# Kernel optimization log

Hardware: AMD Instinct MI355X
Metric: run time of the kernel (lower is better)

Reference implementation:

```python
import jax, jax.numpy as jnp
import numpy as np

N = 100000          # num nodes
NUM_GRAPHS = 64
NEG_SLOPE = 0.2     # PyG GATv2Conv default


def gatv2_layer(x, src, dst, Wl, bl, Wr, br, att, bias, heads, out_ch, concat):
    # x: [N, F_in]; src/dst: [E] (self-loops already included)
    xl = (x @ Wl + bl).reshape(-1, heads, out_ch)   # source transform
    xr = (x @ Wr + br).reshape(-1, heads, out_ch)   # target transform
    m = jax.nn.leaky_relu(xl[src] + xr[dst], NEG_SLOPE)      # [E, H, C]
    alpha = jnp.einsum('ehc,hc->eh', m, att)                 # [E, H]
    # segment softmax over destination nodes
    amax = jax.ops.segment_max(alpha, dst, num_segments=N)
    alpha = jnp.exp(alpha - amax[dst])
    denom = jax.ops.segment_sum(alpha, dst, num_segments=N)
    alpha = alpha / (denom[dst] + 1e-16)
    out = jax.ops.segment_sum(xl[src] * alpha[..., None], dst, num_segments=N)
    out = out.reshape(N, heads * out_ch) if concat else out.mean(axis=1)
    return out + bias


def setup_inputs() -> dict:
    key = jax.random.key(0)
    ks = jax.random.split(key, 16)
    E = 3200000
    x = jax.random.normal(ks[0], (N, 256), dtype=jnp.float32)
    edge_index = jax.random.randint(ks[1], (2, E), 0, N, dtype=jnp.int64)
    batch = jnp.sort(jax.random.randint(ks[2], (N,), 0, NUM_GRAPHS, dtype=jnp.int64))
    H1, C1 = 8, 4
    s1 = 1.0 / np.sqrt(256)
    s2 = 1.0 / np.sqrt(H1 * C1)
    return {
        'x': x, 'edge_index': edge_index, 'batch': batch,
        'W1l': jax.random.normal(ks[3], (256, H1 * C1), jnp.float32) * s1,
        'b1l': jnp.zeros((H1 * C1,), jnp.float32),
        'W1r': jax.random.normal(ks[4], (256, H1 * C1), jnp.float32) * s1,
        'b1r': jnp.zeros((H1 * C1,), jnp.float32),
        'att1': jax.random.normal(ks[5], (H1, C1), jnp.float32),
        'bias1': jnp.zeros((H1 * C1,), jnp.float32),
        'W2l': jax.random.normal(ks[6], (H1 * C1, 64), jnp.float32) * s2,
        'b2l': jnp.zeros((64,), jnp.float32),
        'W2r': jax.random.normal(ks[7], (H1 * C1, 64), jnp.float32) * s2,
        'b2r': jnp.zeros((64,), jnp.float32),
        'att2': jax.random.normal(ks[8], (1, 64), jnp.float32),
        'bias2': jnp.zeros((64,), jnp.float32),
    }


def reference(x, edge_index, batch, W1l, b1l, W1r, b1r, att1, bias1,
              W2l, b2l, W2r, b2r, att2, bias2):
    # add self-loops (PyG GATv2Conv default add_self_loops=True)
    loop = jnp.arange(N, dtype=edge_index.dtype)
    src = jnp.concatenate([edge_index[0], loop])
    dst = jnp.concatenate([edge_index[1], loop])
    h = gatv2_layer(x, src, dst, W1l, b1l, W1r, b1r, att1, bias1, 8, 4, True)
    h = jax.nn.elu(h)
    h = gatv2_layer(h, src, dst, W2l, b2l, W2r, b2r, att2, bias2, 1, 64, False)
    # global mean pool over graphs
    sums = jax.ops.segment_sum(h, batch, num_segments=NUM_GRAPHS)
    counts = jax.ops.segment_sum(jnp.ones((N, 1), h.dtype), batch, num_segments=NUM_GRAPHS)
    return sums / jnp.maximum(counts, 1.0)
```

## Files before the change

kernel.cpp:

```cpp
#include <hip/hip_runtime.h>
#include <math.h>

#define NN 100000
#define EE 3200000
#define ET (EE + NN)
#define NG 64

#define NB 196
#define BWID 512
#define PCHUNK 8192
#define PBLOCKS ((ET + PCHUNK - 1) / PCHUNK)

#define OFF_XL1B  0u
#define OFF_XR1   1600000u
#define OFF_H     4800000u
#define OFF_HL2B  8000000u
#define OFF_HR2   11200000u
#define OFF_BEDGE 8000000u
#define OFF_RP    17600000u
#define OFF_ESRC  17700096u
#define OFF_POOL  21000096u
#define OFF_CNTG  21004192u
#define OFF_BCNT  21004256u
#define OFF_BOFF  21004512u
#define OFF_GCUR  21004768u
#define WS_UNITS  21005024u

__device__ __forceinline__ float lrelu(float v) { return v > 0.0f ? v : 0.2f * v; }

__device__ __forceinline__ unsigned pack_bf2(float a, float b) {
  unsigned ua = __float_as_uint(a), ub = __float_as_uint(b);
  ua = (ua + 0x7FFFu + ((ua >> 16) & 1u)) >> 16;
  ub = (ub + 0x7FFFu + ((ub >> 16) & 1u)) & 0xFFFF0000u;
  return ua | ub;
}
__device__ __forceinline__ float bf_lo(unsigned u) { return __uint_as_float(u << 16); }
__device__ __forceinline__ float bf_hi(unsigned u) { return __uint_as_float(u & 0xFFFF0000u); }

__global__ __launch_bounds__(256) void k_bcount(const int* __restrict__ ei,
                                                int* __restrict__ bcnt) {
  __shared__ int h[NB];
  for (int i = threadIdx.x; i < NB; i += 256) h[i] = 0;
  __syncthreads();
  for (long e = (long)blockIdx.x * 256 + threadIdx.x; e < ET; e += (long)gridDim.x * 256) {
    int d = (e < EE) ? ei[EE + e] : (int)(e - EE);
    atomicAdd(&h[d >> 9], 1);
  }
  __syncthreads();
  for (int i = threadIdx.x; i < NB; i += 256) if (h[i]) atomicAdd(&bcnt[i], h[i]);
}

__global__ __launch_bounds__(256) void k_bscan(const int* __restrict__ bcnt,
                                               int* __restrict__ boff, int* __restrict__ gcur) {
  __shared__ int sd[256];
  int t = threadIdx.x;
  int v = (t < NB) ? bcnt[t] : 0;
  sd[t] = v;
  __syncthreads();
  for (int o = 1; o < 256; o <<= 1) {
    int u = (t >= o) ? sd[t - o] : 0;
    __syncthreads();
    sd[t] += u;
    __syncthreads();
  }
  if (t < NB) { boff[t] = sd[t] - v; gcur[t] = sd[t] - v; }
  if (t == 0) boff[NB] = ET;
}

__global__ __launch_bounds__(512) void k_part(const int* __restrict__ ei,
                                              int* __restrict__ gcur,
                                              int* __restrict__ bedge) {
  __shared__ int  cnt[NB];
  __shared__ int  lbase[NB];
  __shared__ int  gbase[NB];
  __shared__ int  sc[256];
  __shared__ int  buf[PCHUNK];
  __shared__ unsigned char bkt[PCHUNK];
  int tid = threadIdx.x;
  long e0 = (long)blockIdx.x * PCHUNK;
  int nedge = (e0 + PCHUNK <= ET) ? PCHUNK : (int)(ET - e0);

  for (int i = tid; i < NB; i += 512) cnt[i] = 0;
  __syncthreads();
  for (int i = tid; i < nedge; i += 512) {
    long e = e0 + i;
    int d = (e < EE) ? ei[EE + e] : (int)(e - EE);
    atomicAdd(&cnt[d >> 9], 1);
  }
  __syncthreads();
  if (tid < 256) sc[tid] = (tid < NB) ? cnt[tid] : 0;
  __syncthreads();
  for (int o = 1; o < 256; o <<= 1) {
    int u = (tid < 256 && tid >= o) ? sc[tid - o] : 0;
    __syncthreads();
    if (tid < 256) sc[tid] += u;
    __syncthreads();
  }
  if (tid < NB) lbase[tid] = sc[tid] - cnt[tid];
  __syncthreads();
  if (tid < NB) {
    int c = cnt[tid];
    gbase[tid] = c ? atomicAdd(&gcur[tid], c) : 0;
    cnt[tid] = 0;
  }
  __syncthreads();
  for (int i = tid; i < nedge; i += 512) {
    long e = e0 + i;
    int s, d;
    if (e < EE) { s = ei[e]; d = ei[EE + e]; }
    else { s = (int)(e - EE); d = s; }
    int b = d >> 9;
    int r = atomicAdd(&cnt[b], 1);
    int idx = lbase[b] + r;
    buf[idx] = s | ((d & 511) << 17);
    bkt[idx] = (unsigned char)b;
  }
  __syncthreads();
  for (int i = tid; i < nedge; i += 512) {
    int p = buf[i];
    int b = bkt[i];
    bedge[gbase[b] + (i - lbase[b])] = p;
  }
}

__global__ __launch_bounds__(512) void k_csr(const int* __restrict__ boff,
                                             const int* __restrict__ bedge,
                                             int* __restrict__ rp, int* __restrict__ esrc) {
  __shared__ int sdeg[BWID];
  __shared__ int sscan[BWID];
  int b = blockIdx.x, t = threadIdx.x;
  int n0 = b * BWID;
  int lo = boff[b], hi = boff[b + 1];
  sdeg[t] = 0;
  __syncthreads();
  for (int i = lo + t; i < hi; i += 512) {
    int p = bedge[i];
    atomicAdd(&sdeg[p >> 17], 1);
  }
  __syncthreads();
  int v = sdeg[t];
  sscan[t] = v;
  __syncthreads();
  for (int o = 1; o < 512; o <<= 1) {
    int u = (t >= o) ? sscan[t - o] : 0;
    __syncthreads();
    sscan[t] += u;
    __syncthreads();
  }
  int excl = sscan[t] - v;
  int n = n0 + t;
  if (n < NN) rp[n] = lo + excl;
  if (b == NB - 1 && t == 0) rp[NN] = ET;
  __syncthreads();
  sdeg[t] = lo + excl;
  __syncthreads();
  for (int i = lo + t; i < hi; i += 512) {
    int p = bedge[i];
    int pos = atomicAdd(&sdeg[p >> 17], 1);
    esrc[pos] = p & 0x1FFFF;
  }
}

#define FMA4A(a, xv) \
  a.x += xv.x*w0.x + xv.y*w1.x + xv.z*w2.x + xv.w*w3.x; \
  a.y += xv.x*w0.y + xv.y*w1.y + xv.z*w2.y + xv.w*w3.y; \
  a.z += xv.x*w0.z + xv.y*w1.z + xv.z*w2.z + xv.w*w3.z; \
  a.w += xv.x*w0.w + xv.y*w1.w + xv.z*w2.w + xv.w*w3.w;

__global__ __launch_bounds__(256, 4) void k_xform1(
    const float* __restrict__ x,
    const float* __restrict__ Wl, const float* __restrict__ bl,
    const float* __restrict__ Wr, const float* __restrict__ br,
    unsigned short* __restrict__ xl1b, float* __restrict__ xr1) {
  __shared__ float Wlds[64 * 64];
  int tid = threadIdx.x;
  int ci = tid & 15, ni = tid >> 4;
  int cbase = ci * 4;
  int n0 = blockIdx.x * 64 + ni * 4;
  int r0 = n0 + 0 < NN ? n0 + 0 : NN - 1;
  int r1 = n0 + 1 < NN ? n0 + 1 : NN - 1;
  int r2 = n0 + 2 < NN ? n0 + 2 : NN - 1;
  int r3 = n0 + 3 < NN ? n0 + 3 : NN - 1;
  const float* xb0 = x + (size_t)r0 * 256;
  const float* xb1 = x + (size_t)r1 * 256;
  const float* xb2 = x + (size_t)r2 * 256;
  const float* xb3 = x + (size_t)r3 * 256;
  float4 acc0 = {0,0,0,0}, acc1 = {0,0,0,0}, acc2 = {0,0,0,0}, acc3 = {0,0,0,0};

  for (int q = 0; q < 4; ++q) {
    int k0 = q * 64;
    __syncthreads();
    for (int i = tid; i < 64 * 64; i += 256) {
      int k = (i >> 6) + k0, c = i & 63;
      Wlds[i] = (c < 32) ? Wl[k * 32 + c] : Wr[k * 32 + (c - 32)];
    }
    __syncthreads();
#pragma unroll 2
    for (int kk = 0; kk < 64; kk += 4) {
      int k = k0 + kk;
      float4 xv0 = *(const float4*)(xb0 + k);
      float4 xv1 = *(const float4*)(xb1 + k);
      float4 xv2 = *(const float4*)(xb2 + k);
      float4 xv3 = *(const float4*)(xb3 + k);
      const float* wr = &Wlds[kk * 64 + cbase];
      float4 w0 = *(const float4*)(wr);
      float4 w1 = *(const float4*)(wr + 64);
      float4 w2 = *(const float4*)(wr + 128);
      float4 w3 = *(const float4*)(wr + 192);
      FMA4A(acc0, xv0)
      FMA4A(acc1, xv1)
      FMA4A(acc2, xv2)
      FMA4A(acc3, xv3)
    }
  }
  float4 acc[4] = {acc0, acc1, acc2, acc3};
  if (cbase < 32) {
    float4 bv = { bl[cbase], bl[cbase+1], bl[cbase+2], bl[cbase+3] };
#pragma unroll
    for (int j = 0; j < 4; ++j) {
      int n = n0 + j;
      if (n < NN) {
        uint2 o = { pack_bf2(acc[j].x + bv.x, acc[j].y + bv.y),
                    pack_bf2(acc[j].z + bv.z, acc[j].w + bv.w) };
        *(uint2*)(xl1b + (size_t)n * 32 + cbase) = o;
      }
    }
  } else {
    int c2 = cbase - 32;
    float4 bv = { br[c2], br[c2+1], br[c2+2], br[c2+3] };
#pragma unroll
    for (int j = 0; j < 4; ++j) {
      int n = n0 + j;
      if (n < NN) {
        float4 o = { acc[j].x + bv.x, acc[j].y + bv.y, acc[j].z + bv.z, acc[j].w + bv.w };
        *(float4*)(xr1 + (size_t)n * 32 + c2) = o;
      }
    }
  }
}

__global__ __launch_bounds__(256) void k_gather1(
    const int* __restrict__ rp, const int* __restrict__ esrc,
    const unsigned short* __restrict__ xl1b, const float* __restrict__ xr1,
    const float* __restrict__ att1, const float* __restrict__ bias1,
    float* __restrict__ h) {
  int n = blockIdx.x * 8 + (threadIdx.x >> 5);
  if (n >= NN) return;
  int l = threadIdx.x & 31;
  float av = att1[l];
  float xr = xr1[(size_t)n * 32 + l];
  int rpn = rp[n], dg = rp[n + 1] - rpn;
  float acc = 0.0f, den = 0.0f;
  int j = 0;
  for (; j + 4 <= dg; j += 4) {
    int s0 = esrc[rpn + j + 0];
    int s1 = esrc[rpn + j + 1];
    int s2 = esrc[rpn + j + 2];
    int s3 = esrc[rpn + j + 3];
    float x0 = bf_lo(xl1b[(size_t)s0 * 32 + l]);
    float x1 = bf_lo(xl1b[(size_t)s1 * 32 + l]);
    float x2 = bf_lo(xl1b[(size_t)s2 * 32 + l]);
    float x3 = bf_lo(xl1b[(size_t)s3 * 32 + l]);
    float p0 = lrelu(x0 + xr) * av;
    float p1 = lrelu(x1 + xr) * av;
    float p2 = lrelu(x2 + xr) * av;
    float p3 = lrelu(x3 + xr) * av;
    p0 += __shfl_xor(p0, 1); p1 += __shfl_xor(p1, 1);
    p2 += __shfl_xor(p2, 1); p3 += __shfl_xor(p3, 1);
    p0 += __shfl_xor(p0, 2); p1 += __shfl_xor(p1, 2);
    p2 += __shfl_xor(p2, 2); p3 += __shfl_xor(p3, 2);
    float w0 = __expf(p0), w1 = __expf(p1), w2 = __expf(p2), w3 = __expf(p3);
    den += w0 + w1 + w2 + w3;
    acc += w0 * x0 + w1 * x1 + w2 * x2 + w3 * x3;
  }
  for (; j < dg; ++j) {
    int s = esrc[rpn + j];
    float xl = bf_lo(xl1b[(size_t)s * 32 + l]);
    float p = lrelu(xl + xr) * av;
    p += __shfl_xor(p, 1);
    p += __shfl_xor(p, 2);
    float w = __expf(p);
    den += w;
    acc += w * xl;
  }
  float v = acc / (den + 1e-16f) + bias1[l];
  h[(size_t)n * 32 + l] = v > 0.0f ? v : expm1f(v);
}

__global__ __launch_bounds__(256) void k_xform2(
    const float* __restrict__ h,
    const float* __restrict__ Wl, const float* __restrict__ bl,
    const float* __restrict__ Wr, const float* __restrict__ br,
    unsigned short* __restrict__ hl2b, float* __restrict__ hr2) {
  __shared__ float Wlds[32 * 128];
  int tid = threadIdx.x;
  for (int i = tid; i < 32 * 128; i += 256) {
    int k = i >> 7, c = i & 127;
    Wlds[i] = (c < 64) ? Wl[k * 64 + c] : Wr[k * 64 + (c - 64)];
  }
  __syncthreads();
  int ci = tid & 31, ni = tid >> 5;
  int cbase = ci * 4;
  int n0 = blockIdx.x * 32 + ni * 4;
  const float* hb0 = h + (size_t)(n0 + 0) * 32;
  const float* hb1 = h + (size_t)(n0 + 1) * 32;
  const float* hb2 = h + (size_t)(n0 + 2) * 32;
  const float* hb3 = h + (size_t)(n0 + 3) * 32;
  float4 acc0 = {0,0,0,0}, acc1 = {0,0,0,0}, acc2 = {0,0,0,0}, acc3 = {0,0,0,0};
#pragma unroll
  for (int k = 0; k < 32; k += 4) {
    float4 xv0 = *(const float4*)(hb0 + k);
    float4 xv1 = *(const float4*)(hb1 + k);
    float4 xv2 = *(const float4*)(hb2 + k);
    float4 xv3 = *(const float4*)(hb3 + k);
    const float* wr = &Wlds[k * 128 + cbase];
    float4 w0 = *(const float4*)(wr);
    float4 w1 = *(const float4*)(wr + 128);
    float4 w2 = *(const float4*)(wr + 256);
    float4 w3 = *(const float4*)(wr + 384);
    FMA4A(acc0, xv0)
    FMA4A(acc1, xv1)
    FMA4A(acc2, xv2)
    FMA4A(acc3, xv3)
  }
  float4 acc[4] = {acc0, acc1, acc2, acc3};
  if (cbase < 64) {
    float4 bv = { bl[cbase], bl[cbase+1], bl[cbase+2], bl[cbase+3] };
#pragma unroll
    for (int j = 0; j < 4; ++j) {
      uint2 o = { pack_bf2(acc[j].x + bv.x, acc[j].y + bv.y),
                  pack_bf2(acc[j].z + bv.z, acc[j].w + bv.w) };
      *(uint2*)(hl2b + (size_t)(n0 + j) * 64 + cbase) = o;
    }
  } else {
    int c2 = cbase - 64;
    float4 bv = { br[c2], br[c2+1], br[c2+2], br[c2+3] };
#pragma unroll
    for (int j = 0; j < 4; ++j) {
      float4 o = { acc[j].x + bv.x, acc[j].y + bv.y, acc[j].z + bv.z, acc[j].w + bv.w };
      *(float4*)(hr2 + (size_t)(n0 + j) * 64 + c2) = o;
    }
  }
}

__global__ __launch_bounds__(256) void k_gather2(
    const int* __restrict__ rp, const int* __restrict__ esrc,
    const unsigned short* __restrict__ hl2b, const float* __restrict__ hr2,
    const float* __restrict__ att2, const float* __restrict__ bias2,
    const int* __restrict__ batch,
    float* __restrict__ pool, float* __restrict__ cntg) {
  __shared__ float ssum[4][64];
  __shared__ float scnt[4];
  int tid = threadIdx.x;
  int n = (blockIdx.x * 256 + tid) >> 3;
  int l8 = tid & 7;
  int nblk0 = blockIdx.x * 32;
  int gmin = batch[nblk0];
  int gspan = batch[nblk0 + 31] - gmin + 1;
  ssum[tid >> 6][tid & 63] = 0.0f;
  if (tid < 4) scnt[tid] = 0.0f;
  __syncthreads();

  float4 ac0 = *(const float4*)(att2 + l8 * 8);
  float4 ac1 = *(const float4*)(att2 + l8 * 8 + 4);
  float4 bs0 = *(const float4*)(bias2 + l8 * 8);
  float4 bs1 = *(const float4*)(bias2 + l8 * 8 + 4);
  const float4* hrp = (const float4*)(hr2 + (size_t)n * 64 + l8 * 8);
  float4 hr0 = hrp[0], hr1 = hrp[1];
  int rpn = rp[n], dg = rp[n + 1] - rpn;
  float4 a0 = {0,0,0,0}, a1 = {0,0,0,0};
  float den = 0.0f;
  int j = 0;
  for (; j + 2 <= dg; j += 2) {
    int s0 = esrc[rpn + j];
    int s1 = esrc[rpn + j + 1];
    uint4 q0 = *(const uint4*)(hl2b + (size_t)s0 * 64 + l8 * 8);
    uint4 q1 = *(const uint4*)(hl2b + (size_t)s1 * 64 + l8 * 8);
    float4 u0 = { bf_lo(q0.x), bf_hi(q0.x), bf_lo(q0.y), bf_hi(q0.y) };
    float4 u1 = { bf_lo(q0.z), bf_hi(q0.z), bf_lo(q0.w), bf_hi(q0.w) };
    float4 v0 = { bf_lo(q1.x), bf_hi(q1.x), bf_lo(q1.y), bf_hi(q1.y) };
    float4 v1 = { bf_lo(q1.z), bf_hi(q1.z), bf_lo(q1.w), bf_hi(q1.w) };
    float p0 = lrelu(u0.x + hr0.x) * ac0.x + lrelu(u0.y + hr0.y) * ac0.y
             + lrelu(u0.z + hr0.z) * ac0.z + lrelu(u0.w + hr0.w) * ac0.w
             + lrelu(u1.x + hr1.x) * ac1.x + lrelu(u1.y + hr1.y) * ac1.y
             + lrelu(u1.z + hr1.z) * ac1.z + lrelu(u1.w + hr1.w) * ac1.w;
    float p1 = lrelu(v0.x + hr0.x) * ac0.x + lrelu(v0.y + hr0.y) * ac0.y
             + lrelu(v0.z + hr0.z) * ac0.z + lrelu(v0.w + hr0.w) * ac0.w
             + lrelu(v1.x + hr1.x) * ac1.x + lrelu(v1.y + hr1.y) * ac1.y
             + lrelu(v1.z + hr1.z) * ac1.z + lrelu(v1.w + hr1.w) * ac1.w;
    p0 += __shfl_xor(p0, 1); p1 += __shfl_xor(p1, 1);
    p0 += __shfl_xor(p0, 2); p1 += __shfl_xor(p1, 2);
    p0 += __shfl_xor(p0, 4); p1 += __shfl_xor(p1, 4);
    float w0 = __expf(p0), w1 = __expf(p1);
    den += w0 + w1;
    a0.x += w0 * u0.x + w1 * v0.x; a0.y += w0 * u0.y + w1 * v0.y;
    a0.z += w0 * u0.z + w1 * v0.z; a0.w += w0 * u0.w + w1 * v0.w;
    a1.x += w0 * u1.x + w1 * v1.x; a1.y += w0 * u1.y + w1 * v1.y;
    a1.z += w0 * u1.z + w1 * v1.z; a1.w += w0 * u1.w + w1 * v1.w;
  }
  for (; j < dg; ++j) {
    int s = esrc[rpn + j];
    uint4 q0 = *(const uint4*)(hl2b + (size_t)s * 64 + l8 * 8);
    float4 u0 = { bf_lo(q0.x), bf_hi(q0.x), bf_lo(q0.y), bf_hi(q0.y) };
    float4 u1 = { bf_lo(q0.z), bf_hi(q0.z), bf_lo(q0.w), bf_hi(q0.w) };
    float p = lrelu(u0.x + hr0.x) * ac0.x + lrelu(u0.y + hr0.y) * ac0.y
            + lrelu(u0.z + hr0.z) * ac0.z + lrelu(u0.w + hr0.w) * ac0.w
            + lrelu(u1.x + hr1.x) * ac1.x + lrelu(u1.y + hr1.y) * ac1.y
            + lrelu(u1.z + hr1.z) * ac1.z + lrelu(u1.w + hr1.w) * ac1.w;
    p += __shfl_xor(p, 1);
    p += __shfl_xor(p, 2);
    p += __shfl_xor(p, 4);
    float w = __expf(p);
    den += w;
    a0.x += w * u0.x; a0.y += w * u0.y; a0.z += w * u0.z; a0.w += w * u0.w;
    a1.x += w * u1.x; a1.y += w * u1.y; a1.z += w * u1.z; a1.w += w * u1.w;
  }
  float inv = 1.0f / (den + 1e-16f);
  int gi = batch[n] - gmin;
  float* sp = &ssum[gi][l8 * 8];
  atomicAdd(sp + 0, a0.x * inv + bs0.x);
  atomicAdd(sp + 1, a0.y * inv + bs0.y);
  atomicAdd(sp + 2, a0.z * inv + bs0.z);
  atomicAdd(sp + 3, a0.w * inv + bs0.w);
  atomicAdd(sp + 4, a1.x * inv + bs1.x);
  atomicAdd(sp + 5, a1.y * inv + bs1.y);
  atomicAdd(sp + 6, a1.z * inv + bs1.z);
  atomicAdd(sp + 7, a1.w * inv + bs1.w);
  if (l8 == 0) atomicAdd(&scnt[gi], 1.0f);
  __syncthreads();
  for (int i = tid; i < gspan * 64; i += 256)
    atomicAdd(pool + (size_t)(gmin + (i >> 6)) * 64 + (i & 63), ssum[i >> 6][i & 63]);
  if (tid < gspan) atomicAdd(cntg + gmin + tid, scnt[tid]);
}

__global__ __launch_bounds__(256) void k_final(
    const float* __restrict__ pool, const float* __restrict__ cntg,
    float* __restrict__ out) {
  int i = blockIdx.x * 256 + threadIdx.x;
  if (i < NG * 64) out[i] = pool[i] / fmaxf(cntg[i >> 6], 1.0f);
}

extern "C" void kernel_launch(void* const* d_in, const int* in_sizes, int n_in,
                              void* d_out, int out_size, void* d_ws, size_t ws_size,
                              hipStream_t stream) {
  const float* x     = (const float*)d_in[0];
  const int*   ei    = (const int*)d_in[1];
  const int*   batch = (const int*)d_in[2];
  const float* W1l   = (const float*)d_in[3];
  const float* b1l   = (const float*)d_in[4];
  const float* W1r   = (const float*)d_in[5];
  const float* b1r   = (const float*)d_in[6];
  const float* att1  = (const float*)d_in[7];
  const float* bias1 = (const float*)d_in[8];
  const float* W2l   = (const float*)d_in[9];
  const float* b2l   = (const float*)d_in[10];
  const float* W2r   = (const float*)d_in[11];
  const float* b2r   = (const float*)d_in[12];
  const float* att2  = (const float*)d_in[13];
  const float* bias2 = (const float*)d_in[14];
  float* ws = (float*)d_ws;
  int*   wi = (int*)d_ws;
  float* out = (float*)d_out;

  hipMemsetAsync(ws + OFF_POOL, 0, (size_t)(WS_UNITS - OFF_POOL) * 4, stream);

  k_bcount<<<512, 256, 0, stream>>>(ei, wi + OFF_BCNT);
  k_bscan<<<1, 256, 0, stream>>>(wi + OFF_BCNT, wi + OFF_BOFF, wi + OFF_GCUR);
  k_part<<<PBLOCKS, 512, 0, stream>>>(ei, wi + OFF_GCUR, wi + OFF_BEDGE);
  k_csr<<<NB, 512, 0, stream>>>(wi + OFF_BOFF, wi + OFF_BEDGE,
                                wi + OFF_RP, wi + OFF_ESRC);

  k_xform1<<<(NN + 63) / 64, 256, 0, stream>>>(x, W1l, b1l, W1r, b1r,
                                               (unsigned short*)(ws + OFF_XL1B), ws + OFF_XR1);
  k_gather1<<<NN / 8, 256, 0, stream>>>(wi + OFF_RP, wi + OFF_ESRC,
                                        (const unsigned short*)(ws + OFF_XL1B), ws + OFF_XR1,
                                        att1, bias1, ws + OFF_H);
  k_xform2<<<NN / 32, 256, 0, stream>>>(ws + OFF_H, W2l, b2l, W2r, b2r,
                                        (unsigned short*)(ws + OFF_HL2B), ws + OFF_HR2);
  k_gather2<<<(NN * 8 + 255) / 256, 256, 0, stream>>>(wi + OFF_RP, wi + OFF_ESRC,
                                                      (const unsigned short*)(ws + OFF_HL2B),
                                                      ws + OFF_HR2, att2, bias2, batch,
                                                      ws + OFF_POOL, ws + OFF_CNTG);
  k_final<<<16, 256, 0, stream>>>(ws + OFF_POOL, ws + OFF_CNTG, out);
}
```

Baseline: 383.9 us.

## Co-schedule layer-1 transform with CSR build kernels and unroll gather2 by four

Splits the first-layer node transform into two halves and runs them inside the edge-partition and CSR-build kernels as extra blocks, dispatched on block index with dynamic shared memory. The memory-bound dense transform then overlaps with the atomics-heavy graph construction instead of running as a separate launch afterwards. The transform now uses 512-thread blocks covering 128 nodes, and the shared-memory size is set by the larger partition role, which may reduce occupancy. Separately, the layer-2 gather loop is unrolled from two to four edges to expose more independent loads in flight.

Result: faster. 355.7 us (-7.3%).

```diff
diff --git a/kernel.cpp b/kernel.cpp
--- a/kernel.cpp
+++ b/kernel.cpp
@@ -10,6 +10,10 @@
 #define BWID 512
 #define PCHUNK 8192
 #define PBLOCKS ((ET + PCHUNK - 1) / PCHUNK)
+
+#define X1_SPLIT 50048
+#define X1BLK_A 391
+#define X1BLK_B 391
 
 #define OFF_XL1B  0u
 #define OFF_XR1   1600000u
@@ -67,17 +71,16 @@
   if (t == 0) boff[NB] = ET;
 }
 
-__global__ __launch_bounds__(512) void k_part(const int* __restrict__ ei,
-                                              int* __restrict__ gcur,
-                                              int* __restrict__ bedge) {
-  __shared__ int  cnt[NB];
-  __shared__ int  lbase[NB];
-  __shared__ int  gbase[NB];
-  __shared__ int  sc[256];
-  __shared__ int  buf[PCHUNK];
-  __shared__ unsigned char bkt[PCHUNK];
+__device__ void part_role(char* smem, const int* __restrict__ ei,
+                          int* __restrict__ gcur, int* __restrict__ bedge, int pblk) {
+  int* cnt   = (int*)smem;
+  int* lbase = cnt + NB;
+  int* gbase = lbase + NB;
+  int* sc    = gbase + NB;
+  int* buf   = sc + 256;
+  unsigned char* bkt = (unsigned char*)(buf + PCHUNK);
   int tid = threadIdx.x;
-  long e0 = (long)blockIdx.x * PCHUNK;
+  long e0 = (long)pblk * PCHUNK;
   int nedge = (e0 + PCHUNK <= ET) ? PCHUNK : (int)(ET - e0);
 
   for (int i = tid; i < NB; i += 512) cnt[i] = 0;
@@ -123,12 +126,12 @@
   }
 }
 
-__global__ __launch_bounds__(512) void k_csr(const int* __restrict__ boff,
-                                             const int* __restrict__ bedge,
-                                             int* __restrict__ rp, int* __restrict__ esrc) {
-  __shared__ int sdeg[BWID];
-  __shared__ int sscan[BWID];
-  int b = blockIdx.x, t = threadIdx.x;
+__device__ void csr_role(char* smem, const int* __restrict__ boff,
+                         const int* __restrict__ bedge,
+                         int* __restrict__ rp, int* __restrict__ esrc, int b) {
+  int* sdeg  = (int*)smem;
+  int* sscan = sdeg + BWID;
+  int t = threadIdx.x;
   int n0 = b * BWID;
   int lo = boff[b], hi = boff[b + 1];
   sdeg[t] = 0;
@@ -167,16 +170,16 @@
   a.z += xv.x*w0.z + xv.y*w1.z + xv.z*w2.z + xv.w*w3.z; \
   a.w += xv.x*w0.w + xv.y*w1.w + xv.z*w2.w + xv.w*w3.w;
 
-__global__ __launch_bounds__(256, 4) void k_xform1(
-    const float* __restrict__ x,
-    const float* __restrict__ Wl, const float* __restrict__ bl,
-    const float* __restrict__ Wr, const float* __restrict__ br,
-    unsigned short* __restrict__ xl1b, float* __restrict__ xr1) {
-  __shared__ float Wlds[64 * 64];
+__device__ void xform1_role(char* smem, const float* __restrict__ x,
+                            const float* __restrict__ Wl, const float* __restrict__ bl,
+                            const float* __restrict__ Wr, const float* __restrict__ br,
+                            unsigned short* __restrict__ xl1b, float* __restrict__ xr1,
+                            int n_base) {
+  float* Wlds = (float*)smem;
   int tid = threadIdx.x;
-  int ci = tid & 15, ni = tid >> 4;
+  int ci = tid & 15;
   int cbase = ci * 4;
-  int n0 = blockIdx.x * 64 + ni * 4;
+  int n0 = n_base + (tid >> 4) * 4;
   int r0 = n0 + 0 < NN ? n0 + 0 : NN - 1;
   int r1 = n0 + 1 < NN ? n0 + 1 : NN - 1;
   int r2 = n0 + 2 < NN ? n0 + 2 : NN - 1;
@@ -190,7 +193,7 @@
   for (int q = 0; q < 4; ++q) {
     int k0 = q * 64;
     __syncthreads();
-    for (int i = tid; i < 64 * 64; i += 256) {
+    for (int i = tid; i < 64 * 64; i += 512) {
       int k = (i >> 6) + k0, c = i & 63;
       Wlds[i] = (c < 32) ? Wl[k * 32 + c] : Wr[k * 32 + (c - 32)];
     }
@@ -237,6 +240,34 @@
       }
     }
   }
+}
+
+__global__ __launch_bounds__(512) void k_part_x1(
+    const int* __restrict__ ei, int* __restrict__ gcur, int* __restrict__ bedge,
+    const float* __restrict__ x,
+    const float* __restrict__ Wl, const float* __restrict__ bl,
+    const float* __restrict__ Wr, const float* __restrict__ br,
+    unsigned short* __restrict__ xl1b, float* __restrict__ xr1) {
+  extern __shared__ char smem[];
+  if (blockIdx.x < PBLOCKS)
+    part_role(smem, ei, gcur, bedge, blockIdx.x);
+  else
+    xform1_role(smem, x, Wl, bl, Wr, br, xl1b, xr1, (blockIdx.x - PBLOCKS) * 128);
+}
+
+__global__ __launch_bounds__(512) void k_csr_x1(
+    const int* __restrict__ boff, const int* __restrict__ bedge,
+    int* __restrict__ rp, int* __restrict__ esrc,
+    const float* __restrict__ x,
+    const float* __restrict__ Wl, const float* __restrict__ bl,
+    const float* __restrict__ Wr, const float* __restrict__ br,
+    unsigned short* __restrict__ xl1b, float* __restrict__ xr1) {
+  extern __shared__ char smem[];
+  if (blockIdx.x < NB)
+    csr_role(smem, boff, bedge, rp, esrc, blockIdx.x);
+  else
+    xform1_role(smem, x, Wl, bl, Wr, br, xl1b, xr1,
+                X1_SPLIT + (blockIdx.x - NB) * 128);
 }
 
 __global__ __launch_bounds__(256) void k_gather1(
@@ -343,6 +374,20 @@
   }
 }
 
+#define G2_P(qq, pp) { \
+  float4 U0 = { bf_lo(qq.x), bf_hi(qq.x), bf_lo(qq.y), bf_hi(qq.y) }; \
+  float4 U1 = { bf_lo(qq.z), bf_hi(qq.z), bf_lo(qq.w), bf_hi(qq.w) }; \
+  pp = lrelu(U0.x + hr0.x) * ac0.x + lrelu(U0.y + hr0.y) * ac0.y \
+     + lrelu(U0.z + hr0.z) * ac0.z + lrelu(U0.w + hr0.w) * ac0.w \
+     + lrelu(U1.x + hr1.x) * ac1.x + lrelu(U1.y + hr1.y) * ac1.y \
+     + lrelu(U1.z + hr1.z) * ac1.z + lrelu(U1.w + hr1.w) * ac1.w; }
+
+#define G2_ACC(qq, ww) { \
+  float4 U0 = { bf_lo(qq.x), bf_hi(qq.x), bf_lo(qq.y), bf_hi(qq.y) }; \
+  float4 U1 = { bf_lo(qq.z), bf_hi(qq.z), bf_lo(qq.w), bf_hi(qq.w) }; \
+  a0.x += ww * U0.x; a0.y += ww * U0.y; a0.z += ww * U0.z; a0.w += ww * U0.w; \
+  a1.x += ww * U1.x; a1.y += ww * U1.y; a1.z += ww * U1.z; a1.w += ww * U1.w; }
+
 __global__ __launch_bounds__(256) void k_gather2(
     const int* __restrict__ rp, const int* __restrict__ esrc,
     const unsigned short* __restrict__ hl2b, const float* __restrict__ hr2,
@@ -371,49 +416,38 @@
   float4 a0 = {0,0,0,0}, a1 = {0,0,0,0};
   float den = 0.0f;
   int j = 0;
-  for (; j + 2 <= dg; j += 2) {
-    int s0 = esrc[rpn + j];
+  for (; j + 4 <= dg; j += 4) {
+    int s0 = esrc[rpn + j + 0];
     int s1 = esrc[rpn + j + 1];
+    int s2 = esrc[rpn + j + 2];
+    int s3 = esrc[rpn + j + 3];
     uint4 q0 = *(const uint4*)(hl2b + (size_t)s0 * 64 + l8 * 8);
     uint4 q1 = *(const uint4*)(hl2b + (size_t)s1 * 64 + l8 * 8);
-    float4 u0 = { bf_lo(q0.x), bf_hi(q0.x), bf_lo(q0.y), bf_hi(q0.y) };
-    float4 u1 = { bf_lo(q0.z), bf_hi(q0.z), bf_lo(q0.w), bf_hi(q0.w) };
-    float4 v0 = { bf_lo(q1.x), bf_hi(q1.x), bf_lo(q1.y), bf_hi(q1.y) };
-    float4 v1 = { bf_lo(q1.z), bf_hi(q1.z), bf_lo(q1.w), bf_hi(q1.w) };
-    float p0 = lrelu(u0.x + hr0.x) * ac0.x + lrelu(u0.y + hr0.y) * ac0.y
-             + lrelu(u0.z + hr0.z) * ac0.z + lrelu(u0.w + hr0.w) * ac0.w
-             + lrelu(u1.x + hr1.x) * ac1.x + lrelu(u1.y + hr1.y) * ac1.y
-             + lrelu(u1.z + hr1.z) * ac1.z + lrelu(u1.w + hr1.w) * ac1.w;
-    float p1 = lrelu(v0.x + hr0.x) * ac0.x + lrelu(v0.y + hr0.y) * ac0.y
-             + lrelu(v0.z + hr0.z) * ac0.z + lrelu(v0.w + hr0.w) * ac0.w
-             + lrelu(v1.x + hr1.x) * ac1.x + lrelu(v1.y + hr1.y) * ac1.y
-             + lrelu(v1.z + hr1.z) * ac1.z + lrelu(v1.w + hr1.w) * ac1.w;
+    uint4 q2 = *(const uint4*)(hl2b + (size_t)s2 * 64 + l8 * 8);
+    uint4 q3 = *(const uint4*)(hl2b + (size_t)s3 * 64 + l8 * 8);
+    float p0, p1, p2, p3;
+    G2_P(q0, p0) G2_P(q1, p1) G2_P(q2, p2) G2_P(q3, p3)
     p0 += __shfl_xor(p0, 1); p1 += __shfl_xor(p1, 1);
+    p2 += __shfl_xor(p2, 1); p3 += __shfl_xor(p3, 1);
     p0 += __shfl_xor(p0, 2); p1 += __shfl_xor(p1, 2);
+    p2 += __shfl_xor(p2, 2); p3 += __shfl_xor(p3, 2);
     p0 += __shfl_xor(p0, 4); p1 += __shfl_xor(p1, 4);
-    float w0 = __expf(p0), w1 = __expf(p1);
-    den += w0 + w1;
-    a0.x += w0 * u0.x + w1 * v0.x; a0.y += w0 * u0.y + w1 * v0.y;
-    a0.z += w0 * u0.z + w1 * v0.z; a0.w += w0 * u0.w + w1 * v0.w;
-    a1.x += w0 * u1.x + w1 * v1.x; a1.y += w0 * u1.y + w1 * v1.y;
-    a1.z += w0 * u1.z + w1 * v1.z; a1.w += w0 * u1.w + w1 * v1.w;
+    p2 += __shfl_xor(p2, 4); p3 += __shfl_xor(p3, 4);
+    float w0 = __expf(p0), w1 = __expf(p1), w2 = __expf(p2), w3 = __expf(p3);
+    den += w0 + w1 + w2 + w3;
+    G2_ACC(q0, w0) G2_ACC(q1, w1) G2_ACC(q2, w2) G2_ACC(q3, w3)
   }
   for (; j < dg; ++j) {
     int s = esrc[rpn + j];
     uint4 q0 = *(const uint4*)(hl2b + (size_t)s * 64 + l8 * 8);
-    float4 u0 = { bf_lo(q0.x), bf_hi(q0.x), bf_lo(q0.y), bf_hi(q0.y) };
-    float4 u1 = { bf_lo(q0.z), bf_hi(q0.z), bf_lo(q0.w), bf_hi(q0.w) };
-    float p = lrelu(u0.x + hr0.x) * ac0.x + lrelu(u0.y + hr0.y) * ac0.y
-            + lrelu(u0.z + hr0.z) * ac0.z + lrelu(u0.w + hr0.w) * ac0.w
-            + lrelu(u1.x + hr1.x) * ac1.x + lrelu(u1.y + hr1.y) * ac1.y
-            + lrelu(u1.z + hr1.z) * ac1.z + lrelu(u1.w + hr1.w) * ac1.w;
+    float p;
+    G2_P(q0, p)
     p += __shfl_xor(p, 1);
     p += __shfl_xor(p, 2);
     p += __shfl_xor(p, 4);
     float w = __expf(p);
     den += w;
-    a0.x += w * u0.x; a0.y += w * u0.y; a0.z += w * u0.z; a0.w += w * u0.w;
-    a1.x += w * u1.x; a1.y += w * u1.y; a1.z += w * u1.z; a1.w += w * u1.w;
+    G2_ACC(q0, w)
   }
   float inv = 1.0f / (den + 1e-16f);
   int gi = batch[n] - gmin;
@@ -466,12 +500,13 @@
 
   k_bcount<<<512, 256, 0, stream>>>(ei, wi + OFF_BCNT);
   k_bscan<<<1, 256, 0, stream>>>(wi + OFF_BCNT, wi + OFF_BOFF, wi + OFF_GCUR);
-  k_part<<<PBLOCKS, 512, 0, stream>>>(ei, wi + OFF_GCUR, wi + OFF_BEDGE);
-  k_csr<<<NB, 512, 0, stream>>>(wi + OFF_BOFF, wi + OFF_BEDGE,
-                                wi + OFF_RP, wi + OFF_ESRC);
-
-  k_xform1<<<(NN + 63) / 64, 256, 0, stream>>>(x, W1l, b1l, W1r, b1r,
-                                               (unsigned short*)(ws + OFF_XL1B), ws + OFF_XR1);
+  k_part_x1<<<PBLOCKS + X1BLK_A, 512, 44352, stream>>>(
+      ei, wi + OFF_GCUR, wi + OFF_BEDGE,
+      x, W1l, b1l, W1r, b1r, (unsigned short*)(ws + OFF_XL1B), ws + OFF_XR1);
+  k_csr_x1<<<NB + X1BLK_B, 512, 16384, stream>>>(
+      wi + OFF_BOFF, wi + OFF_BEDGE, wi + OFF_RP, wi + OFF_ESRC,
+      x, W1l, b1l, W1r, b1r, (unsigned short*)(ws + OFF_XL1B), ws + OFF_XR1);
+
   k_gather1<<<NN / 8, 256, 0, stream>>>(wi + OFF_RP, wi + OFF_ESRC,
                                         (const unsigned short*)(ws + OFF_XL1B), ws + OFF_XR1,
                                         att1, bias1, ws + OFF_H);
```
